# Optimization experiments

Hardware: AMD Instinct MI355X
Metric: run time of the kernel (lower is better)

Reference implementation:

```python
import jax, jax.numpy as jnp
import numpy as np

N_NODES = 50000
N_EDGES = 800000
NUM_FEATURES = 3
HIDDEN = 128
NUM_GRAPHS = 100
NUM_CLASSES = 2


def setup_inputs() -> dict:
    key = jax.random.key(0)
    ks = jax.random.split(key, 12)
    x = jax.random.normal(ks[0], (N_NODES, NUM_FEATURES), dtype=jnp.float32)
    edge_index = jax.random.randint(ks[1], (2, N_EDGES), 0, N_NODES, dtype=jnp.int64)
    batch = jnp.sort(jax.random.randint(ks[2], (N_NODES,), 0, NUM_GRAPHS, dtype=jnp.int64))
    c1, c2, c3 = 4 * HIDDEN, 2 * HIDDEN, HIDDEN  # 512, 256, 128

    def glorot(k, fan_in, fan_out):
        s = jnp.sqrt(6.0 / (fan_in + fan_out)).astype(jnp.float32)
        return jax.random.uniform(k, (fan_in, fan_out), jnp.float32, -s, s)

    W1 = glorot(ks[3], NUM_FEATURES, c1); b1 = jnp.zeros((c1,), jnp.float32)
    W2 = glorot(ks[4], c1, c2);           b2 = jnp.zeros((c2,), jnp.float32)
    W3 = glorot(ks[5], c2, c3);           b3 = jnp.zeros((c3,), jnp.float32)
    Wc = glorot(ks[6], c3, NUM_CLASSES);  bc = jnp.zeros((NUM_CLASSES,), jnp.float32)
    return {"x": x, "W1": W1, "b1": b1, "W2": W2, "b2": b2, "W3": W3, "b3": b3,
            "Wc": Wc, "bc": bc, "edge_index": edge_index, "batch": batch}


def reference(x, W1, b1, W2, b2, W3, b3, Wc, bc, edge_index, batch):
    n = x.shape[0]
    self_loop = jnp.arange(n, dtype=edge_index.dtype)
    row = jnp.concatenate([edge_index[0], self_loop])  # source nodes (messages from)
    col = jnp.concatenate([edge_index[1], self_loop])  # target nodes (aggregate into)
    # symmetric GCN normalization with self-loops: deg^{-1/2}[row] * deg^{-1/2}[col]
    deg = jax.ops.segment_sum(jnp.ones(row.shape, x.dtype), col, num_segments=n)
    dis = jnp.where(deg > 0, jax.lax.rsqrt(jnp.maximum(deg, 1.0)), 0.0)
    norm = dis[row] * dis[col]  # [E + N]

    def gcn_conv(h, W, b):
        m = h @ W                                   # project first (cheap GEMM)
        agg = jax.ops.segment_sum(norm[:, None] * m[row], col, num_segments=n)
        return agg + b

    h = jax.nn.relu(gcn_conv(x, W1, b1))
    h = jax.nn.relu(gcn_conv(h, W2, b2))
    h = jax.nn.relu(gcn_conv(h, W3, b3))

    # global mean pool over graphs
    counts = jax.ops.segment_sum(jnp.ones((n,), h.dtype), batch, num_segments=NUM_GRAPHS)
    pooled = jax.ops.segment_sum(h, batch, num_segments=NUM_GRAPHS) / jnp.maximum(counts, 1.0)[:, None]

    logits = pooled @ Wc + bc
    return jax.nn.log_softmax(logits, axis=1)
```

## Files before the change

### kernel.cpp

```cpp
#include <hip/hip_runtime.h>
#include <hip/hip_bf16.h>
#include <math.h>

#define N_NODES 50000
#define N_EDGES 800000
#define NFEAT 3
#define C1 512
#define C2 256
#define C3 128
#define NGRAPH 100
#define NCLS 2
#define PSPLIT 8

typedef short bh8 __attribute__((ext_vector_type(8)));
typedef float f32x4 __attribute__((ext_vector_type(4)));

__device__ __forceinline__ short f2bf(float x) {
    __hip_bfloat16 h = __float2bfloat16(x);
    return *reinterpret_cast<short*>(&h);
}
__device__ __forceinline__ float bflo(unsigned int u) { return __uint_as_float(u << 16); }
__device__ __forceinline__ float bfhi(unsigned int u) { return __uint_as_float(u & 0xffff0000u); }


__global__ void count_edges(const int* __restrict__ col, int* __restrict__ counts) {
    int e = blockIdx.x * blockDim.x + threadIdx.x;
    if (e < N_EDGES) atomicAdd(&counts[col[e]], 1);
}


__global__ void scan_chunks(const int* __restrict__ counts, int* __restrict__ offsets,
                            int* __restrict__ chunksums, float* __restrict__ dis) {
    __shared__ int s[256];
    int b = blockIdx.x, t = threadIdx.x;
    int i = b * 256 + t;
    int v = (i < N_NODES) ? counts[i] : 0;
    if (i < N_NODES) dis[i] = rsqrtf((float)(v + 1));
    s[t] = v;
    __syncthreads();
    for (int d = 1; d < 256; d <<= 1) {
        int add = (t >= d) ? s[t - d] : 0;
        __syncthreads();
        s[t] += add;
        __syncthreads();
    }
    if (i < N_NODES) offsets[i + 1] = s[t];
    if (t == 255) chunksums[b] = s[255];
}

__global__ void scan_sums(int* __restrict__ chunksums, int nchunks) {
    __shared__ int s[256];
    int t = threadIdx.x;
    int v = (t < nchunks) ? chunksums[t] : 0;
    s[t] = v;
    __syncthreads();
    for (int d = 1; d < 256; d <<= 1) {
        int add = (t >= d) ? s[t - d] : 0;
        __syncthreads();
        s[t] += add;
        __syncthreads();
    }
    if (t < nchunks) chunksums[t] = (t == 0) ? 0 : s[t - 1];
}

__global__ void finalize_offsets(int* __restrict__ offsets, const int* __restrict__ chunkoffs,
                                 int* __restrict__ cursor) {
    int i = blockIdx.x * blockDim.x + threadIdx.x;
    if (i < N_NODES) {
        int v = offsets[i + 1] + chunkoffs[i / 256];
        offsets[i + 1] = v;
        if (i + 1 < N_NODES) cursor[i + 1] = v;
    }
    if (i == 0) { offsets[0] = 0; cursor[0] = 0; }
}

__global__ void scatter_edges(const int* __restrict__ rowi, const int* __restrict__ coli,
                              int* __restrict__ cursor, int* __restrict__ csr_src) {
    int e = blockIdx.x * blockDim.x + threadIdx.x;
    if (e < N_EDGES) {
        int r = rowi[e], c = coli[e];
        int p = atomicAdd(&cursor[c], 1);
        csr_src[p] = r;
    }
}


__global__ void prep_weights(const float* __restrict__ W2, const float* __restrict__ W3,
                             short* __restrict__ W2t, short* __restrict__ W3t) {
    int idx = blockIdx.x * 256 + threadIdx.x;
    if (idx < C1 * C2) {
        int n = idx / C1, k = idx % C1;
        W2t[idx] = f2bf(W2[k * C2 + n]);
    } else if (idx < C1 * C2 + C2 * C3) {
        int j = idx - C1 * C2;
        int n = j / C2, k = j % C2;
        W3t[j] = f2bf(W3[k * C3 + n]);
    }
}


__global__ void agg_feat3(const float* __restrict__ x, const int* __restrict__ offsets,
                          const int* __restrict__ csr_src, const float* __restrict__ dis,
                          float* __restrict__ aggx) {
    int i = blockIdx.x * blockDim.x + threadIdx.x;
    if (i >= N_NODES) return;
    float di = dis[i];
    float a0 = di * x[i * 3 + 0], a1 = di * x[i * 3 + 1], a2 = di * x[i * 3 + 2];
    int s = offsets[i], e = offsets[i + 1];
    int p = s;
    for (; p + 4 <= e; p += 4) {
        int r0 = csr_src[p], r1 = csr_src[p + 1], r2 = csr_src[p + 2], r3 = csr_src[p + 3];
        float d0 = dis[r0], d1 = dis[r1], d2 = dis[r2], d3 = dis[r3];
        float3 v0 = *(const float3*)&x[r0 * 3];
        float3 v1 = *(const float3*)&x[r1 * 3];
        float3 v2 = *(const float3*)&x[r2 * 3];
        float3 v3 = *(const float3*)&x[r3 * 3];
        a0 += d0 * v0.x + d1 * v1.x + d2 * v2.x + d3 * v3.x;
        a1 += d0 * v0.y + d1 * v1.y + d2 * v2.y + d3 * v3.y;
        a2 += d0 * v0.z + d1 * v1.z + d2 * v2.z + d3 * v3.z;
    }
    for (; p < e; ++p) {
        int r = csr_src[p];
        float dr = dis[r];
        a0 += dr * x[r * 3 + 0];
        a1 += dr * x[r * 3 + 1];
        a2 += dr * x[r * 3 + 2];
    }
    aggx[i * 3 + 0] = di * a0; aggx[i * 3 + 1] = di * a1; aggx[i * 3 + 2] = di * a2;
}

#define L1_NB 16
__global__ __launch_bounds__(256) void layer1(const float* __restrict__ aggx,
                                              const float* __restrict__ W1,
                                              const float* __restrict__ b1,
                                              const float* __restrict__ dis,
                                              short* __restrict__ h1) {
    __shared__ float sW[3 * C1];
    __shared__ float sb[C1];
    __shared__ float sa[L1_NB * 3];
    __shared__ float sd[L1_NB];
    int t = threadIdx.x;
    int base = blockIdx.x * L1_NB;
    for (int j = t; j < 3 * C1; j += 256) sW[j] = W1[j];
    for (int j = t; j < C1; j += 256) sb[j] = b1[j];
    if (t < L1_NB * 3) sa[t] = aggx[base * 3 + t];
    if (t < L1_NB) sd[t] = dis[base + t];
    __syncthreads();
    int j0 = 2 * t, j1 = 2 * t + 1;
    float w00 = sW[j0], w01 = sW[C1 + j0], w02 = sW[2 * C1 + j0];
    float w10 = sW[j1], w11 = sW[C1 + j1], w12 = sW[2 * C1 + j1];
    float bb0 = sb[j0], bb1 = sb[j1];
    unsigned int* h1u = (unsigned int*)h1;
#pragma unroll
    for (int n = 0; n < L1_NB; ++n) {
        int i = base + n;
        float a0 = sa[n * 3], a1 = sa[n * 3 + 1], a2 = sa[n * 3 + 2], di = sd[n];
        float v0 = di * fmaxf(a0 * w00 + a1 * w01 + a2 * w02 + bb0, 0.f);
        float v1 = di * fmaxf(a0 * w10 + a1 * w11 + a2 * w12 + bb1, 0.f);
        unsigned int pk = (unsigned int)(unsigned short)f2bf(v0) |
                          ((unsigned int)(unsigned short)f2bf(v1) << 16);
        h1u[(size_t)i * (C1 / 2) + t] = pk;
    }
}


template <int K, int BN>
__global__ __launch_bounds__(512, 4) void gemm_bf16(const short* __restrict__ A,
                                                    const short* __restrict__ Bt,
                                                    short* __restrict__ Cmat, int M) {
    __shared__ short As[128 * 32];
    __shared__ short Bs[BN * 32];
    constexpr int NT = BN / 64;
    int bm = blockIdx.x * 128;
    int t = threadIdx.x;
    int wave = t >> 6, lane = t & 63, quad = lane >> 4, l16 = lane & 15;
    int wm = (wave >> 2) * 64;
    int wn = (wave & 3) * (BN / 4);
    f32x4 acc[4][NT] = {};

    int ar = t >> 2, ak = (t & 3) * 8;
    int agr = bm + ar; if (agr > M - 1) agr = M - 1;
    const short* aptr = A + (size_t)agr * K + ak;

    for (int k0 = 0; k0 < K; k0 += 32) {
        *(bh8*)&As[ar * 32 + ak] = *(const bh8*)(aptr + k0);
        if constexpr (BN == 256) {
            int br = t >> 1, bk = (t & 1) * 16;
            const short* bptr = Bt + (size_t)br * K + bk + k0;
            *(bh8*)&Bs[br * 32 + bk]     = *(const bh8*)bptr;
            *(bh8*)&Bs[br * 32 + bk + 8] = *(const bh8*)(bptr + 8);
        } else {
            int br = t >> 2, bk = (t & 3) * 8;
            *(bh8*)&Bs[br * 32 + bk] = *(const bh8*)(Bt + (size_t)br * K + bk + k0);
        }
        __syncthreads();
        bh8 af[4], bf[NT];
#pragma unroll
        for (int mt = 0; mt < 4; ++mt)
            af[mt] = *(const bh8*)&As[(wm + mt * 16 + l16) * 32 + quad * 8];
#pragma unroll
        for (int nt = 0; nt < NT; ++nt)
            bf[nt] = *(const bh8*)&Bs[(wn + nt * 16 + l16) * 32 + quad * 8];
#pragma unroll
        for (int mt = 0; mt < 4; ++mt)
#pragma unroll
            for (int nt = 0; nt < NT; ++nt)
                acc[mt][nt] = __builtin_amdgcn_mfma_f32_16x16x32_bf16(af[mt], bf[nt], acc[mt][nt], 0, 0, 0);
        __syncthreads();
    }

#pragma unroll
    for (int mt = 0; mt < 4; ++mt)
#pragma unroll
        for (int nt = 0; nt < NT; ++nt) {
            int colc = wn + nt * 16 + l16;
#pragma unroll
            for (int r = 0; r < 4; ++r) {
                int rowc = bm + wm + mt * 16 + quad * 4 + r;
                if (rowc < M) Cmat[(size_t)rowc * BN + colc] = f2bf(acc[mt][nt][r]);
            }
        }
}


template <int C, bool PRESCALE>
__global__ void aggregate_ns(const short* __restrict__ m, const int* __restrict__ offsets,
                             const int* __restrict__ csr_src, const float* __restrict__ dis,
                             const float* __restrict__ bias, short* __restrict__ out) {
    int i = blockIdx.x;
    int t = threadIdx.x;
    float di = dis[i];
    const unsigned int* mu = (const unsigned int*)m;
    unsigned int v = mu[(size_t)i * (C / 2) + t];
    float acc0 = bflo(v), acc1 = bfhi(v);
    int s = offsets[i], e = offsets[i + 1];
    int p = s;
    for (; p + 8 <= e; p += 8) {
        int r0 = csr_src[p],     r1 = csr_src[p + 1], r2 = csr_src[p + 2], r3 = csr_src[p + 3];
        int r4 = csr_src[p + 4], r5 = csr_src[p + 5], r6 = csr_src[p + 6], r7 = csr_src[p + 7];
        unsigned int u0 = mu[(size_t)r0 * (C / 2) + t];
        unsigned int u1 = mu[(size_t)r1 * (C / 2) + t];
        unsigned int u2 = mu[(size_t)r2 * (C / 2) + t];
        unsigned int u3 = mu[(size_t)r3 * (C / 2) + t];
        unsigned int u4 = mu[(size_t)r4 * (C / 2) + t];
        unsigned int u5 = mu[(size_t)r5 * (C / 2) + t];
        unsigned int u6 = mu[(size_t)r6 * (C / 2) + t];
        unsigned int u7 = mu[(size_t)r7 * (C / 2) + t];
        acc0 += bflo(u0) + bflo(u1) + bflo(u2) + bflo(u3) +
                bflo(u4) + bflo(u5) + bflo(u6) + bflo(u7);
        acc1 += bfhi(u0) + bfhi(u1) + bfhi(u2) + bfhi(u3) +
                bfhi(u4) + bfhi(u5) + bfhi(u6) + bfhi(u7);
    }
    for (; p < e; ++p) {
        int r = csr_src[p];
        unsigned int u = mu[(size_t)r * (C / 2) + t];
        acc0 += bflo(u);
        acc1 += bfhi(u);
    }
    acc0 = fmaxf(di * acc0 + bias[2 * t], 0.f);
    acc1 = fmaxf(di * acc1 + bias[2 * t + 1], 0.f);
    if (PRESCALE) { acc0 *= di; acc1 *= di; }
    unsigned int pk = (unsigned int)(unsigned short)f2bf(acc0) |
                      ((unsigned int)(unsigned short)f2bf(acc1) << 16);
    ((unsigned int*)out)[(size_t)i * (C / 2) + t] = pk;
}


__global__ void pool_partial(const short* __restrict__ h3, const int* __restrict__ batch,
                             float* __restrict__ pooled) {
    int g = blockIdx.x, sp = blockIdx.y;
    int t = threadIdx.x;
    __shared__ int seg[2];
    if (t < 2) {
        int target = g + t;
        int lo = 0, hi = N_NODES;
        while (lo < hi) { int mid = (lo + hi) >> 1; if (batch[mid] < target) lo = mid + 1; else hi = mid; }
        seg[t] = lo;
    }
    __syncthreads();
    int start = seg[0], end = seg[1];
    int len = end - start;
    int chunk = (len + PSPLIT - 1) / PSPLIT;
    int a = start + sp * chunk;
    int b = a + chunk; if (b > end) b = end;
    if (a >= b) return;
    const unsigned int* hu = (const unsigned int*)h3;
    float s0 = 0.f, s1 = 0.f;
    int i = a;
    for (; i + 4 <= b; i += 4) {
        unsigned int u0 = hu[(size_t)(i + 0) * (C3 / 2) + t];
        unsigned int u1 = hu[(size_t)(i + 1) * (C3 / 2) + t];
        unsigned int u2 = hu[(size_t)(i + 2) * (C3 / 2) + t];
        unsigned int u3 = hu[(size_t)(i + 3) * (C3 / 2) + t];
        s0 += bflo(u0) + bflo(u1) + bflo(u2) + bflo(u3);
        s1 += bfhi(u0) + bfhi(u1) + bfhi(u2) + bfhi(u3);
    }
    for (; i < b; ++i) {
        unsigned int u = hu[(size_t)i * (C3 / 2) + t];
        s0 += bflo(u);
        s1 += bfhi(u);
    }
    atomicAdd(&pooled[g * C3 + 2 * t], s0);
    atomicAdd(&pooled[g * C3 + 2 * t + 1], s1);
}


__global__ void finalize_head(const float* __restrict__ pooled, const int* __restrict__ batch,
                              const float* __restrict__ Wc, const float* __restrict__ bc,
                              float* __restrict__ outp) {
    int g = blockIdx.x;
    int t = threadIdx.x;
    __shared__ int seg[2];
    if (t < 2) {
        int target = g + t;
        int lo = 0, hi = N_NODES;
        while (lo < hi) { int mid = (lo + hi) >> 1; if (batch[mid] < target) lo = mid + 1; else hi = mid; }
        seg[t] = lo;
    }
    __syncthreads();
    float cnt = (float)(seg[1] - seg[0]);
    float pv = pooled[(size_t)g * C3 + t] / fmaxf(cnt, 1.f);
    float p0 = pv * Wc[t * 2 + 0];
    float p1 = pv * Wc[t * 2 + 1];
#pragma unroll
    for (int o = 32; o > 0; o >>= 1) {
        p0 += __shfl_down(p0, o);
        p1 += __shfl_down(p1, o);
    }
    __shared__ float r0[2], r1[2];
    int wid = t >> 6, lane = t & 63;
    if (lane == 0) { r0[wid] = p0; r1[wid] = p1; }
    __syncthreads();
    if (t == 0) {
        float l0 = r0[0] + r0[1] + bc[0];
        float l1 = r1[0] + r1[1] + bc[1];
        float mx = fmaxf(l0, l1);
        float lse = mx + logf(expf(l0 - mx) + expf(l1 - mx));
        outp[g * 2 + 0] = l0 - lse;
        outp[g * 2 + 1] = l1 - lse;
    }
}


extern "C" void kernel_launch(void* const* d_in, const int* in_sizes, int n_in,
                              void* d_out, int out_size, void* d_ws, size_t ws_size,
                              hipStream_t stream) {
    const float* x = (const float*)d_in[0];
    const float* W1 = (const float*)d_in[1];
    const float* b1 = (const float*)d_in[2];
    const float* W2 = (const float*)d_in[3];
    const float* b2 = (const float*)d_in[4];
    const float* W3 = (const float*)d_in[5];
    const float* b3 = (const float*)d_in[6];
    const float* Wc = (const float*)d_in[7];
    const float* bc = (const float*)d_in[8];
    const int* ei = (const int*)d_in[9];
    const int* batch = (const int*)d_in[10];
    const int* row = ei;
    const int* col = ei + N_EDGES;
    float* out = (float*)d_out;

    char* ws = (char*)d_ws;
    size_t off = 0;
    auto alloc = [&](size_t bytes) -> void* {
        off = (off + 255) & ~(size_t)255;
        void* p = ws + off;
        off += bytes;
        return p;
    };

    int* counts = (int*)alloc((size_t)N_NODES * 4);
    int* offsets = (int*)alloc((size_t)(N_NODES + 1) * 4);
    int* cursor = (int*)alloc((size_t)N_NODES * 4);
    int* chunksums = (int*)alloc(256 * 4);
    float* dis = (float*)alloc((size_t)N_NODES * 4);
    int* csr_src = (int*)alloc((size_t)N_EDGES * 4);
    float* aggx = (float*)alloc((size_t)N_NODES * 3 * 4);
    short* W2t = (short*)alloc((size_t)C1 * C2 * 2);
    short* W3t = (short*)alloc((size_t)C2 * C3 * 2);
    short* h1 = (short*)alloc((size_t)N_NODES * C1 * 2);
    short* m2 = (short*)alloc((size_t)N_NODES * C2 * 2);
    short* h2 = (short*)alloc((size_t)N_NODES * C2 * 2);
    short* m3 = (short*)alloc((size_t)N_NODES * C3 * 2);
    short* h3 = (short*)alloc((size_t)N_NODES * C3 * 2);
    float* pooled = (float*)alloc((size_t)NGRAPH * C3 * 4);

    hipMemsetAsync(counts, 0, (size_t)N_NODES * 4, stream);
    hipMemsetAsync(pooled, 0, (size_t)NGRAPH * C3 * 4, stream);
    count_edges<<<(N_EDGES + 255) / 256, 256, 0, stream>>>(col, counts);
    int nchunks = (N_NODES + 255) / 256;
    scan_chunks<<<nchunks, 256, 0, stream>>>(counts, offsets, chunksums, dis);
    scan_sums<<<1, 256, 0, stream>>>(chunksums, nchunks);
    finalize_offsets<<<(N_NODES + 255) / 256, 256, 0, stream>>>(offsets, chunksums, cursor);
    scatter_edges<<<(N_EDGES + 255) / 256, 256, 0, stream>>>(row, col, cursor, csr_src);

    prep_weights<<<(C1 * C2 + C2 * C3 + 255) / 256, 256, 0, stream>>>(W2, W3, W2t, W3t);

    agg_feat3<<<(N_NODES + 255) / 256, 256, 0, stream>>>(x, offsets, csr_src, dis, aggx);
    layer1<<<N_NODES / L1_NB, 256, 0, stream>>>(aggx, W1, b1, dis, h1);

    gemm_bf16<C1, C2><<<(N_NODES + 127) / 128, 512, 0, stream>>>(h1, W2t, m2, N_NODES);
    aggregate_ns<C2, true><<<N_NODES, C2 / 2, 0, stream>>>(m2, offsets, csr_src, dis, b2, h2);

    gemm_bf16<C2, C3><<<(N_NODES + 127) / 128, 512, 0, stream>>>(h2, W3t, m3, N_NODES);
    aggregate_ns<C3, false><<<N_NODES, C3 / 2, 0, stream>>>(m3, offsets, csr_src, dis, b3, h3);

    dim3 gp(NGRAPH, PSPLIT);
    pool_partial<<<gp, C3 / 2, 0, stream>>>(h3, batch, pooled);
    finalize_head<<<NGRAPH, C3, 0, stream>>>(pooled, batch, Wc, bc, out);
}
```

Baseline: 336.8 us.

## Store GEMM output in 32-column slices and aggregate per slice

The GEMM epilogue now writes its output in a column-sliced layout, with 32 bf16 columns (64 bytes) per slice stored contiguously across all nodes. The aggregation kernel is rewritten so that each block handles one slice for two nodes. Within a wave, four edge groups gather 16-lane chunks in parallel and are combined with cross-lane shuffles. The aim is a small working set per slice for better L2 locality during the random gathers, plus more edge-level parallelism, at the cost of 64-byte gather granularity, extra blocks and GEMM stores that now stride by 64 bytes.

```diff
diff --git a/kernel.cpp b/kernel.cpp
--- a/kernel.cpp
+++ b/kernel.cpp
@@ -21,6 +21,9 @@
 }
 __device__ __forceinline__ float bflo(unsigned int u) { return __uint_as_float(u << 16); }
 __device__ __forceinline__ float bfhi(unsigned int u) { return __uint_as_float(u & 0xffff0000u); }
+__device__ __forceinline__ unsigned int packbf(float a, float b) {
+    return (unsigned int)(unsigned short)f2bf(a) | ((unsigned int)(unsigned short)f2bf(b) << 16);
+}
 
 
 __global__ void count_edges(const int* __restrict__ col, int* __restrict__ counts) {
@@ -157,9 +160,7 @@
         float a0 = sa[n * 3], a1 = sa[n * 3 + 1], a2 = sa[n * 3 + 2], di = sd[n];
         float v0 = di * fmaxf(a0 * w00 + a1 * w01 + a2 * w02 + bb0, 0.f);
         float v1 = di * fmaxf(a0 * w10 + a1 * w11 + a2 * w12 + bb1, 0.f);
-        unsigned int pk = (unsigned int)(unsigned short)f2bf(v0) |
-                          ((unsigned int)(unsigned short)f2bf(v1) << 16);
-        h1u[(size_t)i * (C1 / 2) + t] = pk;
+        h1u[(size_t)i * (C1 / 2) + t] = packbf(v0, v1);
     }
 }
 
@@ -214,55 +215,64 @@
 #pragma unroll
         for (int nt = 0; nt < NT; ++nt) {
             int colc = wn + nt * 16 + l16;
+            size_t sb = ((size_t)(colc >> 5) * N_NODES) * 32 + (colc & 31);
 #pragma unroll
             for (int r = 0; r < 4; ++r) {
                 int rowc = bm + wm + mt * 16 + quad * 4 + r;
-                if (rowc < M) Cmat[(size_t)rowc * BN + colc] = f2bf(acc[mt][nt][r]);
+                if (rowc < M) Cmat[sb + (size_t)rowc * 32] = f2bf(acc[mt][nt][r]);
             }
         }
 }
 
 
-template <int C, bool PRESCALE>
-__global__ void aggregate_ns(const short* __restrict__ m, const int* __restrict__ offsets,
-                             const int* __restrict__ csr_src, const float* __restrict__ dis,
-                             const float* __restrict__ bias, short* __restrict__ out) {
-    int i = blockIdx.x;
-    int t = threadIdx.x;
-    float di = dis[i];
+template <int NS, bool PRESCALE>
+__global__ __launch_bounds__(128) void aggregate_sl(const short* __restrict__ m,
+        const int* __restrict__ offsets, const int* __restrict__ csr_src,
+        const float* __restrict__ dis, const float* __restrict__ bias,
+        short* __restrict__ out) {
+    int slice = blockIdx.x % NS;
+    int wave = threadIdx.x >> 6, lane = threadIdx.x & 63;
+    int i = (blockIdx.x / NS) * 2 + wave;
+    int eo = lane >> 4;
+    int c = lane & 15;
     const unsigned int* mu = (const unsigned int*)m;
-    unsigned int v = mu[(size_t)i * (C / 2) + t];
-    float acc0 = bflo(v), acc1 = bfhi(v);
+    size_t sbase = (size_t)slice * N_NODES * 16;
+    float a0 = 0.f, a1 = 0.f;
+    if (eo == 0) {
+        unsigned int v = mu[sbase + (size_t)i * 16 + c];
+        a0 = bflo(v); a1 = bfhi(v);
+    }
     int s = offsets[i], e = offsets[i + 1];
     int p = s;
-    for (; p + 8 <= e; p += 8) {
-        int r0 = csr_src[p],     r1 = csr_src[p + 1], r2 = csr_src[p + 2], r3 = csr_src[p + 3];
-        int r4 = csr_src[p + 4], r5 = csr_src[p + 5], r6 = csr_src[p + 6], r7 = csr_src[p + 7];
-        unsigned int u0 = mu[(size_t)r0 * (C / 2) + t];
-        unsigned int u1 = mu[(size_t)r1 * (C / 2) + t];
-        unsigned int u2 = mu[(size_t)r2 * (C / 2) + t];
-        unsigned int u3 = mu[(size_t)r3 * (C / 2) + t];
-        unsigned int u4 = mu[(size_t)r4 * (C / 2) + t];
-        unsigned int u5 = mu[(size_t)r5 * (C / 2) + t];
-        unsigned int u6 = mu[(size_t)r6 * (C / 2) + t];
-        unsigned int u7 = mu[(size_t)r7 * (C / 2) + t];
-        acc0 += bflo(u0) + bflo(u1) + bflo(u2) + bflo(u3) +
-                bflo(u4) + bflo(u5) + bflo(u6) + bflo(u7);
-        acc1 += bfhi(u0) + bfhi(u1) + bfhi(u2) + bfhi(u3) +
-                bfhi(u4) + bfhi(u5) + bfhi(u6) + bfhi(u7);
-    }
-    for (; p < e; ++p) {
-        int r = csr_src[p];
-        unsigned int u = mu[(size_t)r * (C / 2) + t];
-        acc0 += bflo(u);
-        acc1 += bfhi(u);
-    }
-    acc0 = fmaxf(di * acc0 + bias[2 * t], 0.f);
-    acc1 = fmaxf(di * acc1 + bias[2 * t + 1], 0.f);
-    if (PRESCALE) { acc0 *= di; acc1 *= di; }
-    unsigned int pk = (unsigned int)(unsigned short)f2bf(acc0) |
-                      ((unsigned int)(unsigned short)f2bf(acc1) << 16);
-    ((unsigned int*)out)[(size_t)i * (C / 2) + t] = pk;
+    for (; p + 16 <= e; p += 16) {
+        int r0 = __builtin_nontemporal_load(&csr_src[p + eo]);
+        int r1 = __builtin_nontemporal_load(&csr_src[p + 4 + eo]);
+        int r2 = __builtin_nontemporal_load(&csr_src[p + 8 + eo]);
+        int r3 = __builtin_nontemporal_load(&csr_src[p + 12 + eo]);
+        unsigned int u0 = mu[sbase + (size_t)r0 * 16 + c];
+        unsigned int u1 = mu[sbase + (size_t)r1 * 16 + c];
+        unsigned int u2 = mu[sbase + (size_t)r2 * 16 + c];
+        unsigned int u3 = mu[sbase + (size_t)r3 * 16 + c];
+        a0 += bflo(u0) + bflo(u1) + bflo(u2) + bflo(u3);
+        a1 += bfhi(u0) + bfhi(u1) + bfhi(u2) + bfhi(u3);
+    }
+    for (; p < e; p += 4) {
+        int q = p + eo;
+        if (q < e) {
+            int r = __builtin_nontemporal_load(&csr_src[q]);
+            unsigned int u = mu[sbase + (size_t)r * 16 + c];
+            a0 += bflo(u); a1 += bfhi(u);
+        }
+    }
+    a0 += __shfl_xor(a0, 16); a0 += __shfl_xor(a0, 32);
+    a1 += __shfl_xor(a1, 16); a1 += __shfl_xor(a1, 32);
+    if (eo == 0) {
+        float di = dis[i];
+        a0 = fmaxf(di * a0 + bias[slice * 32 + 2 * c], 0.f);
+        a1 = fmaxf(di * a1 + bias[slice * 32 + 2 * c + 1], 0.f);
+        if (PRESCALE) { a0 *= di; a1 *= di; }
+        ((unsigned int*)out)[(size_t)i * (NS * 16) + slice * 16 + c] = packbf(a0, a1);
+    }
 }
 
 
@@ -400,10 +410,10 @@
     layer1<<<N_NODES / L1_NB, 256, 0, stream>>>(aggx, W1, b1, dis, h1);
 
     gemm_bf16<C1, C2><<<(N_NODES + 127) / 128, 512, 0, stream>>>(h1, W2t, m2, N_NODES);
-    aggregate_ns<C2, true><<<N_NODES, C2 / 2, 0, stream>>>(m2, offsets, csr_src, dis, b2, h2);
+    aggregate_sl<8, true><<<(N_NODES / 2) * 8, 128, 0, stream>>>(m2, offsets, csr_src, dis, b2, h2);
 
     gemm_bf16<C2, C3><<<(N_NODES + 127) / 128, 512, 0, stream>>>(h2, W3t, m3, N_NODES);
-    aggregate_ns<C3, false><<<N_NODES, C3 / 2, 0, stream>>>(m3, offsets, csr_src, dis, b3, h3);
+    aggregate_sl<4, false><<<(N_NODES / 2) * 4, 128, 0, stream>>>(m3, offsets, csr_src, dis, b3, h3);
 
     dim3 gp(NGRAPH, PSPLIT);
     pool_partial<<<gp, C3 / 2, 0, stream>>>(h3, batch, pooled);
```

After: 538.4 us. 1.6x slower.

## Fuse layer-1 projection into the layer-2 GEMM, computing A tiles on the fly

Applied to the files above, without the earlier changes.

Drops the separate layer1 kernel and the 50000x512 bf16 h1 buffer. The new GEMM builds each A tile in shared memory directly from the 3-feature aggregate, W1, bias, ReLU and the dis prescale, then runs MFMA against W2. This removes a large global write and read of h1 in exchange for redundant ALU work in the GEMM main loop, with no prefetch overlap. Shared memory per block also grows, which may lower occupancy.

```diff
diff --git a/kernel.cpp b/kernel.cpp
--- a/kernel.cpp
+++ b/kernel.cpp
@@ -21,6 +21,9 @@
 }
 __device__ __forceinline__ float bflo(unsigned int u) { return __uint_as_float(u << 16); }
 __device__ __forceinline__ float bfhi(unsigned int u) { return __uint_as_float(u & 0xffff0000u); }
+__device__ __forceinline__ unsigned int packbf(float a, float b) {
+    return (unsigned int)(unsigned short)f2bf(a) | ((unsigned int)(unsigned short)f2bf(b) << 16);
+}
 
 
 __global__ void count_edges(const int* __restrict__ col, int* __restrict__ counts) {
@@ -129,38 +132,80 @@
     aggx[i * 3 + 0] = di * a0; aggx[i * 3 + 1] = di * a1; aggx[i * 3 + 2] = di * a2;
 }
 
-#define L1_NB 16
-__global__ __launch_bounds__(256) void layer1(const float* __restrict__ aggx,
-                                              const float* __restrict__ W1,
-                                              const float* __restrict__ b1,
-                                              const float* __restrict__ dis,
-                                              short* __restrict__ h1) {
-    __shared__ float sW[3 * C1];
-    __shared__ float sb[C1];
-    __shared__ float sa[L1_NB * 3];
-    __shared__ float sd[L1_NB];
-    int t = threadIdx.x;
-    int base = blockIdx.x * L1_NB;
-    for (int j = t; j < 3 * C1; j += 256) sW[j] = W1[j];
-    for (int j = t; j < C1; j += 256) sb[j] = b1[j];
-    if (t < L1_NB * 3) sa[t] = aggx[base * 3 + t];
-    if (t < L1_NB) sd[t] = dis[base + t];
-    __syncthreads();
-    int j0 = 2 * t, j1 = 2 * t + 1;
-    float w00 = sW[j0], w01 = sW[C1 + j0], w02 = sW[2 * C1 + j0];
-    float w10 = sW[j1], w11 = sW[C1 + j1], w12 = sW[2 * C1 + j1];
-    float bb0 = sb[j0], bb1 = sb[j1];
-    unsigned int* h1u = (unsigned int*)h1;
-#pragma unroll
-    for (int n = 0; n < L1_NB; ++n) {
-        int i = base + n;
-        float a0 = sa[n * 3], a1 = sa[n * 3 + 1], a2 = sa[n * 3 + 2], di = sd[n];
-        float v0 = di * fmaxf(a0 * w00 + a1 * w01 + a2 * w02 + bb0, 0.f);
-        float v1 = di * fmaxf(a0 * w10 + a1 * w11 + a2 * w12 + bb1, 0.f);
-        unsigned int pk = (unsigned int)(unsigned short)f2bf(v0) |
-                          ((unsigned int)(unsigned short)f2bf(v1) << 16);
-        h1u[(size_t)i * (C1 / 2) + t] = pk;
-    }
+
+__global__ __launch_bounds__(512, 4) void gemm_l1(const float* __restrict__ aggx,
+                                                  const float* __restrict__ W1,
+                                                  const float* __restrict__ b1,
+                                                  const float* __restrict__ dis,
+                                                  const short* __restrict__ Bt,
+                                                  short* __restrict__ Cmat, int M) {
+    __shared__ short As[128 * 32];
+    __shared__ short Bs[C2 * 32];
+    __shared__ float sW1[3 * C1];
+    __shared__ float sb1[C1];
+    __shared__ float sa[128 * 3];
+    __shared__ float sd[128];
+    int bm = blockIdx.x * 128;
+    int t = threadIdx.x;
+    int wave = t >> 6, lane = t & 63, quad = lane >> 4, l16 = lane & 15;
+    int wm = (wave >> 2) * 64;
+    int wn = (wave & 3) * 64;
+    f32x4 acc[4][4] = {};
+
+    for (int j = t; j < 3 * C1; j += 512) sW1[j] = W1[j];
+    if (t < C1) sb1[t] = b1[t];
+    if (t < 128 * 3) {
+        int r = bm + t / 3; if (r > M - 1) r = M - 1;
+        sa[t] = aggx[r * 3 + (t % 3)];
+    }
+    if (t < 128) {
+        int r = bm + t; if (r > M - 1) r = M - 1;
+        sd[t] = dis[r];
+    }
+    __syncthreads();
+
+    int ar = t >> 2, ak = (t & 3) * 8;
+    int br = t >> 1, bk = (t & 1) * 16;
+    float a0 = sa[ar * 3 + 0], a1 = sa[ar * 3 + 1], a2 = sa[ar * 3 + 2];
+    float drow = sd[ar];
+
+    for (int k0 = 0; k0 < C1; k0 += 32) {
+#pragma unroll
+        for (int j = 0; j < 8; ++j) {
+            int k = k0 + ak + j;
+            float v = a0 * sW1[k] + a1 * sW1[C1 + k] + a2 * sW1[2 * C1 + k] + sb1[k];
+            As[ar * 32 + ak + j] = f2bf(drow * fmaxf(v, 0.f));
+        }
+        const short* bptr = Bt + (size_t)br * C1 + bk + k0;
+        *(bh8*)&Bs[br * 32 + bk]     = *(const bh8*)bptr;
+        *(bh8*)&Bs[br * 32 + bk + 8] = *(const bh8*)(bptr + 8);
+        __syncthreads();
+        bh8 af[4], bf[4];
+#pragma unroll
+        for (int mt = 0; mt < 4; ++mt)
+            af[mt] = *(const bh8*)&As[(wm + mt * 16 + l16) * 32 + quad * 8];
+#pragma unroll
+        for (int nt = 0; nt < 4; ++nt)
+            bf[nt] = *(const bh8*)&Bs[(wn + nt * 16 + l16) * 32 + quad * 8];
+#pragma unroll
+        for (int mt = 0; mt < 4; ++mt)
+#pragma unroll
+            for (int nt = 0; nt < 4; ++nt)
+                acc[mt][nt] = __builtin_amdgcn_mfma_f32_16x16x32_bf16(af[mt], bf[nt], acc[mt][nt], 0, 0, 0);
+        __syncthreads();
+    }
+
+#pragma unroll
+    for (int mt = 0; mt < 4; ++mt)
+#pragma unroll
+        for (int nt = 0; nt < 4; ++nt) {
+            int colc = wn + nt * 16 + l16;
+#pragma unroll
+            for (int r = 0; r < 4; ++r) {
+                int rowc = bm + wm + mt * 16 + quad * 4 + r;
+                if (rowc < M) Cmat[(size_t)rowc * C2 + colc] = f2bf(acc[mt][nt][r]);
+            }
+        }
 }
 
 
@@ -260,9 +305,7 @@
     acc0 = fmaxf(di * acc0 + bias[2 * t], 0.f);
     acc1 = fmaxf(di * acc1 + bias[2 * t + 1], 0.f);
     if (PRESCALE) { acc0 *= di; acc1 *= di; }
-    unsigned int pk = (unsigned int)(unsigned short)f2bf(acc0) |
-                      ((unsigned int)(unsigned short)f2bf(acc1) << 16);
-    ((unsigned int*)out)[(size_t)i * (C / 2) + t] = pk;
+    ((unsigned int*)out)[(size_t)i * (C / 2) + t] = packbf(acc0, acc1);
 }
 
 
@@ -378,7 +421,6 @@
     float* aggx = (float*)alloc((size_t)N_NODES * 3 * 4);
     short* W2t = (short*)alloc((size_t)C1 * C2 * 2);
     short* W3t = (short*)alloc((size_t)C2 * C3 * 2);
-    short* h1 = (short*)alloc((size_t)N_NODES * C1 * 2);
     short* m2 = (short*)alloc((size_t)N_NODES * C2 * 2);
     short* h2 = (short*)alloc((size_t)N_NODES * C2 * 2);
     short* m3 = (short*)alloc((size_t)N_NODES * C3 * 2);
@@ -397,9 +439,8 @@
     prep_weights<<<(C1 * C2 + C2 * C3 + 255) / 256, 256, 0, stream>>>(W2, W3, W2t, W3t);
 
     agg_feat3<<<(N_NODES + 255) / 256, 256, 0, stream>>>(x, offsets, csr_src, dis, aggx);
-    layer1<<<N_NODES / L1_NB, 256, 0, stream>>>(aggx, W1, b1, dis, h1);
-
-    gemm_bf16<C1, C2><<<(N_NODES + 127) / 128, 512, 0, stream>>>(h1, W2t, m2, N_NODES);
+
+    gemm_l1<<<(N_NODES + 127) / 128, 512, 0, stream>>>(aggx, W1, b1, dis, W2t, m2, N_NODES);
     aggregate_ns<C2, true><<<N_NODES, C2 / 2, 0, stream>>>(m2, offsets, csr_src, dis, b2, h2);
 
     gemm_bf16<C2, C3><<<(N_NODES + 127) / 128, 512, 0, stream>>>(h2, W3t, m3, N_NODES);
```

Result: no change. 338.8 us (+0.6%).
